# Performance work log

Measured on AMD Instinct MI355X. Metric: run time of the kernel, lower is better.

Reference implementation:

```python
import jax, jax.numpy as jnp
import numpy as np

B, N, D, Y = 4, 2048, 512, 8921


def setup_inputs() -> dict:
    key = jax.random.key(0)
    ks = jax.random.split(key, 9)
    scale = 1.0 / np.sqrt(D)
    return {
        "x": jax.random.normal(ks[0], (B, N, D), jnp.float32),
        "target": (jax.random.uniform(ks[1], (B, Y), jnp.float32) > 0.98).astype(jnp.float32),
        "y_flow": jax.random.normal(ks[2], (B, Y), jnp.float32),
        "U_w": jax.random.normal(ks[3], (Y, D), jnp.float32) * scale,
        "Ug_w": jax.random.normal(ks[4], (Y, D), jnp.float32) * scale,
        "final_w": jax.random.normal(ks[5], (Y, D), jnp.float32) * scale,
        "final_b": jax.random.normal(ks[6], (Y,), jnp.float32) * scale,
        "gate_w": jax.random.normal(ks[7], (D,), jnp.float32) * scale,
        "gate_b": jax.random.normal(ks[8], (), jnp.float32) * scale,
    }


def reference(x, target, y_flow, U_w, Ug_w, final_w, final_b, gate_w, gate_b):
    # Label attention branch: alpha = softmax(U_w @ x^T) over tokens -> [B, Y, N]
    alpha = jax.nn.softmax(jnp.einsum("yd,bnd->byn", U_w, x), axis=-1)
    m = jnp.einsum("byn,bnd->byd", alpha, x)  # [B, Y, D]

    # Gate attention branch
    alpha_g = jax.nn.softmax(jnp.einsum("yd,bnd->byn", Ug_w, x), axis=-1)
    m_g = jnp.einsum("byn,bnd->byd", alpha_g, x)  # [B, Y, D]

    # gate = tanh(Linear(D,1)(m_gate)) -> [B, Y]
    gate = jnp.tanh(jnp.einsum("byd,d->by", m_g, gate_w) + gate_b)

    # y = sum_d(final_w * m) + final_b + y_flow * gate
    y = jnp.einsum("yd,byd->by", final_w, m) + final_b + y_flow * gate

    # BCEWithLogitsLoss (mean): logaddexp(0, y) - y * target, numerically stable
    loss = jnp.mean(jnp.logaddexp(0.0, y) - y * target)
    return (y, loss)
```

## Files before the change

kernel.cpp:

```cpp
#include <hip/hip_runtime.h>
#include <stdint.h>

#define BQ 4
#define NQ 2048
#define DQ 512
#define YQ 8921
#define YGRP 140
#define NH 4
#define NCHQ 32
#define NUNITS (YGRP * BQ * NH)
#define NLP 140
#define GXOFF 65536
#define L2E 1.44269504088896340736f

typedef __attribute__((ext_vector_type(8))) short bf16x8;
typedef __attribute__((ext_vector_type(4))) float f32x4;

__device__ inline short f2bf(float f) {
  unsigned u = __float_as_uint(f);
  u += 0x7fffu + ((u >> 16) & 1u);
  return (short)(u >> 16);
}

__device__ inline bf16x8 pack8(float4 a, float4 b) {
  bf16x8 h;
  h[0] = f2bf(a.x); h[1] = f2bf(a.y); h[2] = f2bf(a.z); h[3] = f2bf(a.w);
  h[4] = f2bf(b.x); h[5] = f2bf(b.y); h[6] = f2bf(b.z); h[7] = f2bf(b.w);
  return h;
}

__device__ inline void gl_lds16(const void* g, void* l) {
  __builtin_amdgcn_global_load_lds((const __attribute__((address_space(1))) void*)g,
                                   (__attribute__((address_space(3))) void*)l, 16, 0, 0);
}

__global__ __launch_bounds__(256) void prep_gx(const float* __restrict__ x,
                                               const float* __restrict__ gate_w,
                                               float* __restrict__ gx) {
  int rid = blockIdx.x * 4 + (threadIdx.x >> 6);
  int lane = threadIdx.x & 63;
  const float* src = x + (size_t)rid * DQ + lane * 8;
  float4 v0 = *(const float4*)src;
  float4 v1 = *(const float4*)(src + 4);
  const float* gwp = gate_w + lane * 8;
  float s = v0.x * gwp[0] + v0.y * gwp[1] + v0.z * gwp[2] + v0.w * gwp[3]
          + v1.x * gwp[4] + v1.y * gwp[5] + v1.z * gwp[6] + v1.w * gwp[7];
#pragma unroll
  for (int d = 1; d < 64; d <<= 1) s += __shfl_xor(s, d);
  if (lane == 0) gx[rid] = s;
}

__global__ __launch_bounds__(256) void prep_xfrag(const float* __restrict__ x,
                                                  const float* __restrict__ gate_w,
                                                  char* __restrict__ ws_x2,
                                                  float* __restrict__ gx) {
  __shared__ float xs[16 * 512];
  int t = blockIdx.x;
  const float* src = x + ((size_t)t << 13);
  int tid = threadIdx.x;
#pragma unroll
  for (int i = 0; i < 8; ++i)
    *(float4*)(xs + i * 1024 + tid * 4) = *(const float4*)(src + i * 1024 + tid * 4);
  __syncthreads();
  char* dst = ws_x2 + ((size_t)t << 14);
#pragma unroll
  for (int i = 0; i < 4; ++i) {
    int s = i * 256 + tid;
    int l = s & 63, kk = s >> 6;
    int row = l & 15, g = l >> 4;
    const float* p = xs + row * 512 + kk * 32 + g * 8;
    *(bf16x8*)(dst + s * 16) = pack8(*(const float4*)p, *(const float4*)(p + 4));
  }
  int row = tid >> 4, sub = tid & 15;
  const float* xr = xs + row * 512 + sub * 32;
  const float* gw = gate_w + sub * 32;
  float s = 0.f;
#pragma unroll
  for (int i = 0; i < 8; ++i) {
    float4 a = *(const float4*)(xr + i * 4);
    float4 g = *(const float4*)(gw + i * 4);
    s += a.x * g.x + a.y * g.y + a.z * g.z + a.w * g.w;
  }
  s += __shfl_xor(s, 1); s += __shfl_xor(s, 2);
  s += __shfl_xor(s, 4); s += __shfl_xor(s, 8);
  if (sub == 0) gx[t * 16 + row] = s;
}

__global__ __launch_bounds__(256) void prep_w(const float* __restrict__ Uw,
                                              const float* __restrict__ Gw,
                                              const float* __restrict__ Fw,
                                              char* __restrict__ ws_w) {
  int rid = blockIdx.x * 4 + (threadIdx.x >> 6);
  if (rid >= 3 * YQ) return;
  int lane = threadIdx.x & 63;
  int mat = rid / YQ, y = rid % YQ;
  const float* src = (mat == 0 ? Uw : (mat == 1 ? Gw : Fw)) + (size_t)y * DQ + lane * 8;
  *(bf16x8*)(ws_w + (size_t)rid * 1024 + lane * 16) =
      pack8(*(const float4*)src, *(const float4*)(src + 4));
}

template<bool FULL>
__global__ __launch_bounds__(256, 2) void fused_kernel(
    const float* __restrict__ x, const char* __restrict__ ws_x2,
    const char* __restrict__ ws_w,
    const float* __restrict__ Uw, const float* __restrict__ Gw,
    const float* __restrict__ Fw, const float* __restrict__ gx,
    float4* __restrict__ ws_state) {
  extern __shared__ char smem[];
  const int tid = threadIdx.x, l = tid & 63, w = tid >> 6;
  const int lr = l & 15, lg4 = l >> 4;
  int u = (blockIdx.x & 7) * (NUNITS / 8) + (blockIdx.x >> 3);
  const int b = u / (YGRP * NH);
  const int r0 = u % (YGRP * NH);
  const int yg = r0 / NH, nh = r0 % NH;
  const int ybase = yg * 64 + w * 16;
  const int nbase = nh * (NQ / NH);

  bf16x8 wU[16], wG[16], wF[16];
  {
    int y = ybase + lr; if (y >= YQ) y = YQ - 1;
    if constexpr (FULL) {
      const char* p0 = ws_w + ((size_t)y * DQ + lg4 * 8) * 2;
#pragma unroll
      for (int kk = 0; kk < 16; ++kk) {
        wU[kk] = *(const bf16x8*)(p0 + kk * 64);
        wG[kk] = *(const bf16x8*)(p0 + (size_t)YQ * 1024 + kk * 64);
        wF[kk] = *(const bf16x8*)(p0 + (size_t)YQ * 2048 + kk * 64);
      }
    } else {
      const float* pu = Uw + (size_t)y * DQ + lg4 * 8;
      const float* pg = Gw + (size_t)y * DQ + lg4 * 8;
      const float* pf = Fw + (size_t)y * DQ + lg4 * 8;
#pragma unroll
      for (int kk = 0; kk < 16; ++kk) {
        wU[kk] = pack8(*(const float4*)(pu + kk * 32), *(const float4*)(pu + kk * 32 + 4));
        wG[kk] = pack8(*(const float4*)(pg + kk * 32), *(const float4*)(pg + kk * 32 + 4));
        wF[kk] = pack8(*(const float4*)(pf + kk * 32), *(const float4*)(pf + kk * 32 + 4));
      }
    }
  }

  float lU = 0.f, aU = 0.f, lG = 0.f, aG = 0.f;

  if constexpr (FULL) {
    *(float2*)(smem + GXOFF + tid * 8) = *(const float2*)(gx + b * NQ + nbase + tid * 2);
    const char* xb = ws_x2 + (((size_t)(b * 128 + nh * 32)) << 14);
    auto stage = [&](int c) {
      const char* src = xb + ((size_t)c << 14);
      char* lb = smem + (c & 3) * 16384;
#pragma unroll
      for (int j = 0; j < 4; ++j) {
        int s = w * 4 + j;
        gl_lds16(src + s * 1024 + l * 16, lb + s * 1024);
      }
    };
    auto mfma_only = [&](int c, f32x4& sU, f32x4& sG, f32x4& sF) {
      const char* ab = smem + (c & 3) * 16384 + l * 16;
#pragma unroll
      for (int r = 0; r < 4; ++r) { sU[r] = 0.f; sG[r] = 0.f; sF[r] = 0.f; }
      __builtin_amdgcn_s_setprio(1);
#pragma unroll
      for (int kk = 0; kk < 16; ++kk) {
        bf16x8 a = *(const bf16x8*)(ab + kk * 1024);
        sU = __builtin_amdgcn_mfma_f32_16x16x32_bf16(a, wU[kk], sU, 0, 0, 0);
        sG = __builtin_amdgcn_mfma_f32_16x16x32_bf16(a, wG[kk], sG, 0, 0, 0);
        sF = __builtin_amdgcn_mfma_f32_16x16x32_bf16(a, wF[kk], sF, 0, 0, 0);
      }
      __builtin_amdgcn_s_setprio(0);
    };
    auto tail = [&](int c, const f32x4& sU, const f32x4& sG, const f32x4& sF) {
      float4 gxv = *(const float4*)(smem + GXOFF + c * 64 + lg4 * 16);
      float gv[4] = {gxv.x, gxv.y, gxv.z, gxv.w};
#pragma unroll
      for (int r = 0; r < 4; ++r) {
        float eu = __builtin_amdgcn_exp2f(sU[r] * L2E);
        lU += eu; aU = fmaf(eu, sF[r], aU);
        float eg = __builtin_amdgcn_exp2f(sG[r] * L2E);
        lG += eg; aG = fmaf(eg, gv[r], aG);
      }
    };

    __syncthreads();
    stage(0); stage(1);
    asm volatile("s_waitcnt vmcnt(4)" ::: "memory");
    __builtin_amdgcn_s_barrier();

    f32x4 pU, pG, pF, qU, qG, qF;
    mfma_only(0, pU, pG, pF);

#pragma unroll 1
    for (int cp = 0; cp < 15; ++cp) {
      const int c0 = 2 * cp;
      stage(c0 + 2); stage(c0 + 3);
      asm volatile("s_waitcnt vmcnt(8)" ::: "memory");
      __builtin_amdgcn_sched_barrier(0);
      __builtin_amdgcn_s_barrier();
      mfma_only(c0 + 1, qU, qG, qF);
      tail(c0, pU, pG, pF);
      asm volatile("s_waitcnt vmcnt(4)" ::: "memory");
      __builtin_amdgcn_sched_barrier(0);
      __builtin_amdgcn_s_barrier();
      mfma_only(c0 + 2, pU, pG, pF);
      tail(c0 + 1, qU, qG, qF);
    }
    asm volatile("s_waitcnt vmcnt(0)" ::: "memory");
    __builtin_amdgcn_sched_barrier(0);
    __builtin_amdgcn_s_barrier();
    mfma_only(31, qU, qG, qF);
    tail(30, pU, pG, pF);
    tail(31, qU, qG, qF);
  } else {
    const float* gxb = gx + b * NQ + nbase + lg4 * 4;
    for (int c = 0; c < NCHQ; ++c) {
      __syncthreads();
#pragma unroll
      for (int j = 0; j < 4; ++j) {
        int slot = j * 256 + tid;
        int kk = slot >> 6, l2 = slot & 63;
        int row = l2 & 15, g4 = l2 >> 4;
        const float* g = x + ((size_t)(b * NQ + nbase + c * 16 + row)) * DQ
                       + kk * 32 + g4 * 8;
        *(bf16x8*)(smem + slot * 16) = pack8(*(const float4*)g, *(const float4*)(g + 4));
      }
      __syncthreads();
      const char* ab = smem + l * 16;
      f32x4 sU = {0.f, 0.f, 0.f, 0.f}, sG = sU, sF = sU;
#pragma unroll
      for (int kk = 0; kk < 16; ++kk) {
        bf16x8 a = *(const bf16x8*)(ab + kk * 1024);
        sU = __builtin_amdgcn_mfma_f32_16x16x32_bf16(a, wU[kk], sU, 0, 0, 0);
        sG = __builtin_amdgcn_mfma_f32_16x16x32_bf16(a, wG[kk], sG, 0, 0, 0);
        sF = __builtin_amdgcn_mfma_f32_16x16x32_bf16(a, wF[kk], sF, 0, 0, 0);
      }
      float4 gxv = *(const float4*)(gxb + c * 16);
      float gv[4] = {gxv.x, gxv.y, gxv.z, gxv.w};
#pragma unroll
      for (int r = 0; r < 4; ++r) {
        float eu = __builtin_amdgcn_exp2f(sU[r] * L2E);
        lU += eu; aU = fmaf(eu, sF[r], aU);
        float eg = __builtin_amdgcn_exp2f(sG[r] * L2E);
        lG += eg; aG = fmaf(eg, gv[r], aG);
      }
    }
  }

#pragma unroll
  for (int d = 16; d < 64; d <<= 1) {
    lU += __shfl_xor(lU, d); aU += __shfl_xor(aU, d);
    lG += __shfl_xor(lG, d); aG += __shfl_xor(aG, d);
  }

  int y = ybase + lr;
  if (lg4 == 0 && y < YQ) {
    float4 st; st.x = lU; st.y = aU; st.z = lG; st.w = aG;
    ws_state[(size_t)(b * NH + nh) * YQ + y] = st;
  }
}

__global__ __launch_bounds__(256) void merge_kernel(
    const float4* __restrict__ ws_state, const float* __restrict__ fb,
    const float* __restrict__ gate_b, const float* __restrict__ yflow,
    const float* __restrict__ target, float* __restrict__ out_y,
    float* __restrict__ loss_part) {
  __shared__ float sb[256];
  int t = blockIdx.x * 256 + threadIdx.x;
  float lt = 0.f;
  if (t < BQ * YQ) {
    int b = t / YQ, y = t % YQ;
    float lU = 0.f, aU = 0.f, lG = 0.f, aG = 0.f;
#pragma unroll
    for (int nh = 0; nh < NH; ++nh) {
      float4 s = ws_state[(size_t)(b * NH + nh) * YQ + y];
      lU += s.x; aU += s.y; lG += s.z; aG += s.w;
    }
    float gate = tanhf(aG / lG + gate_b[0]);
    float yv = aU / lU + fb[y] + yflow[t] * gate;
    out_y[t] = yv;
    float tg = target[t];
    lt = fmaxf(yv, 0.f) + log1pf(__expf(-fabsf(yv))) - yv * tg;
  }
  sb[threadIdx.x] = lt;
  __syncthreads();
  for (int st = 128; st > 0; st >>= 1) {
    if (threadIdx.x < st) sb[threadIdx.x] += sb[threadIdx.x + st];
    __syncthreads();
  }
  if (threadIdx.x == 0) loss_part[blockIdx.x] = sb[0];
}

__global__ __launch_bounds__(256) void loss_kernel(const float* __restrict__ lp,
                                                   float* __restrict__ out) {
  __shared__ float sb[256];
  float s = (threadIdx.x < NLP) ? lp[threadIdx.x] : 0.f;
  sb[threadIdx.x] = s;
  __syncthreads();
  for (int st = 128; st > 0; st >>= 1) {
    if (threadIdx.x < st) sb[threadIdx.x] += sb[threadIdx.x + st];
    __syncthreads();
  }
  if (threadIdx.x == 0) out[BQ * YQ] = sb[0] / (float)(BQ * YQ);
}

extern "C" void kernel_launch(void* const* d_in, const int* in_sizes, int n_in,
                              void* d_out, int out_size, void* d_ws, size_t ws_size,
                              hipStream_t stream) {
  const float* x      = (const float*)d_in[0];
  const float* target = (const float*)d_in[1];
  const float* yflow  = (const float*)d_in[2];
  const float* Uw     = (const float*)d_in[3];
  const float* Gw     = (const float*)d_in[4];
  const float* Fw     = (const float*)d_in[5];
  const float* fb     = (const float*)d_in[6];
  const float* gw     = (const float*)d_in[7];
  const float* gb     = (const float*)d_in[8];
  float* out = (float*)d_out;
  char* ws = (char*)d_ws;

  const size_t xbytes  = (size_t)BQ * NQ * DQ * 2;
  const size_t wbytes  = (size_t)3 * YQ * DQ * 2;
  const size_t gxbytes = (size_t)BQ * NQ * 4;
  const size_t stbytes = (size_t)BQ * NH * YQ * 16;
  const size_t lpbytes = (size_t)NLP * 4;
  const bool full = ws_size >= xbytes + wbytes + gxbytes + stbytes + lpbytes;

  char* ws_x2; char* ws_w; float* gxp; float4* stp; float* lp;
  if (full) {
    ws_x2 = ws; ws_w = ws + xbytes;
    gxp = (float*)(ws + xbytes + wbytes);
    stp = (float4*)(ws + xbytes + wbytes + gxbytes);
    lp  = (float*)(ws + xbytes + wbytes + gxbytes + stbytes);
  } else {
    ws_x2 = nullptr; ws_w = nullptr;
    gxp = (float*)ws;
    stp = (float4*)(ws + gxbytes);
    lp  = (float*)(ws + gxbytes + stbytes);
  }

  (void)hipFuncSetAttribute(reinterpret_cast<const void*>(&fused_kernel<true>),
                            hipFuncAttributeMaxDynamicSharedMemorySize, 67584);
  (void)hipFuncSetAttribute(reinterpret_cast<const void*>(&fused_kernel<false>),
                            hipFuncAttributeMaxDynamicSharedMemorySize, 16384);

  if (full) {
    prep_xfrag<<<dim3(BQ * 128), 256, 0, stream>>>(x, gw, ws_x2, gxp);
    prep_w<<<dim3((3 * YQ + 3) / 4), 256, 0, stream>>>(Uw, Gw, Fw, ws_w);
    fused_kernel<true ><<<dim3(NUNITS), 256, 67584, stream>>>(
        x, ws_x2, ws_w, Uw, Gw, Fw, gxp, stp);
  } else {
    prep_gx<<<dim3(2048), 256, 0, stream>>>(x, gw, gxp);
    fused_kernel<false><<<dim3(NUNITS), 256, 16384, stream>>>(
        x, ws_x2, ws_w, Uw, Gw, Fw, gxp, stp);
  }
  merge_kernel<<<dim3(NLP), 256, 0, stream>>>(stp, fb, gb, yflow, target, out, lp);
  loss_kernel<<<1, 256, 0, stream>>>(lp, out);
}
```

Baseline: 219.7 us.

## Double per-wave label tile, halve token split, and drop weight prep kernel

Each wave now holds two 16-label tiles (128 labels per block) of register-resident U/Ug/final weights and reuses each shared-memory x fragment across six MFMAs, while the token range is split eight ways instead of four. The separate bf16 weight-conversion kernel is removed and weights are converted from fp32 inline when loaded. The double-buffered MFMA/tail software pipeline is replaced by a simpler loop with prefetch two chunks ahead. The aim is to cut x traffic per label and one launch, at the cost of double the weight registers, occupancy lowered to one block per CU, and less overlap between MFMA and exp work.

Measured after the change: 810.3 us. 3.69x slower.

```diff
diff --git a/kernel.cpp b/kernel.cpp
--- a/kernel.cpp
+++ b/kernel.cpp
@@ -5,9 +5,9 @@
 #define NQ 2048
 #define DQ 512
 #define YQ 8921
-#define YGRP 140
-#define NH 4
-#define NCHQ 32
+#define YGRP 70
+#define NH 8
+#define NCHQ 16
 #define NUNITS (YGRP * BQ * NH)
 #define NLP 140
 #define GXOFF 65536
@@ -86,23 +86,9 @@
   if (sub == 0) gx[t * 16 + row] = s;
 }
 
-__global__ __launch_bounds__(256) void prep_w(const float* __restrict__ Uw,
-                                              const float* __restrict__ Gw,
-                                              const float* __restrict__ Fw,
-                                              char* __restrict__ ws_w) {
-  int rid = blockIdx.x * 4 + (threadIdx.x >> 6);
-  if (rid >= 3 * YQ) return;
-  int lane = threadIdx.x & 63;
-  int mat = rid / YQ, y = rid % YQ;
-  const float* src = (mat == 0 ? Uw : (mat == 1 ? Gw : Fw)) + (size_t)y * DQ + lane * 8;
-  *(bf16x8*)(ws_w + (size_t)rid * 1024 + lane * 16) =
-      pack8(*(const float4*)src, *(const float4*)(src + 4));
-}
-
 template<bool FULL>
-__global__ __launch_bounds__(256, 2) void fused_kernel(
+__global__ __launch_bounds__(256, 1) void fused_kernel(
     const float* __restrict__ x, const char* __restrict__ ws_x2,
-    const char* __restrict__ ws_w,
     const float* __restrict__ Uw, const float* __restrict__ Gw,
     const float* __restrict__ Fw, const float* __restrict__ gx,
     float4* __restrict__ ws_state) {
@@ -113,38 +99,32 @@
   const int b = u / (YGRP * NH);
   const int r0 = u % (YGRP * NH);
   const int yg = r0 / NH, nh = r0 % NH;
-  const int ybase = yg * 64 + w * 16;
+  const int ybase = yg * 128 + w * 32;
   const int nbase = nh * (NQ / NH);
 
-  bf16x8 wU[16], wG[16], wF[16];
-  {
-    int y = ybase + lr; if (y >= YQ) y = YQ - 1;
-    if constexpr (FULL) {
-      const char* p0 = ws_w + ((size_t)y * DQ + lg4 * 8) * 2;
-#pragma unroll
-      for (int kk = 0; kk < 16; ++kk) {
-        wU[kk] = *(const bf16x8*)(p0 + kk * 64);
-        wG[kk] = *(const bf16x8*)(p0 + (size_t)YQ * 1024 + kk * 64);
-        wF[kk] = *(const bf16x8*)(p0 + (size_t)YQ * 2048 + kk * 64);
-      }
-    } else {
-      const float* pu = Uw + (size_t)y * DQ + lg4 * 8;
-      const float* pg = Gw + (size_t)y * DQ + lg4 * 8;
-      const float* pf = Fw + (size_t)y * DQ + lg4 * 8;
-#pragma unroll
-      for (int kk = 0; kk < 16; ++kk) {
-        wU[kk] = pack8(*(const float4*)(pu + kk * 32), *(const float4*)(pu + kk * 32 + 4));
-        wG[kk] = pack8(*(const float4*)(pg + kk * 32), *(const float4*)(pg + kk * 32 + 4));
-        wF[kk] = pack8(*(const float4*)(pf + kk * 32), *(const float4*)(pf + kk * 32 + 4));
-      }
-    }
-  }
-
-  float lU = 0.f, aU = 0.f, lG = 0.f, aG = 0.f;
+  bf16x8 wU[2][16], wG[2][16], wF[2][16];
+#pragma unroll
+  for (int t = 0; t < 2; ++t) {
+    int y = ybase + t * 16 + lr; if (y >= YQ) y = YQ - 1;
+    const float* pu = Uw + (size_t)y * DQ + lg4 * 8;
+    const float* pg = Gw + (size_t)y * DQ + lg4 * 8;
+    const float* pf = Fw + (size_t)y * DQ + lg4 * 8;
+#pragma unroll
+    for (int kk = 0; kk < 16; ++kk) {
+      wU[t][kk] = pack8(*(const float4*)(pu + kk * 32), *(const float4*)(pu + kk * 32 + 4));
+      wG[t][kk] = pack8(*(const float4*)(pg + kk * 32), *(const float4*)(pg + kk * 32 + 4));
+      wF[t][kk] = pack8(*(const float4*)(pf + kk * 32), *(const float4*)(pf + kk * 32 + 4));
+    }
+  }
+
+  float lU0 = 0.f, aU0 = 0.f, lG0 = 0.f, aG0 = 0.f;
+  float lU1 = 0.f, aU1 = 0.f, lG1 = 0.f, aG1 = 0.f;
 
   if constexpr (FULL) {
-    *(float2*)(smem + GXOFF + tid * 8) = *(const float2*)(gx + b * NQ + nbase + tid * 2);
-    const char* xb = ws_x2 + (((size_t)(b * 128 + nh * 32)) << 14);
+    ((float*)(smem + GXOFF))[tid] = gx[b * NQ + nbase + tid];
+    __syncthreads();
+
+    const char* xb = ws_x2 + (((size_t)(b * 128 + nh * NCHQ)) << 14);
     auto stage = [&](int c) {
       const char* src = xb + ((size_t)c << 14);
       char* lb = smem + (c & 3) * 16384;
@@ -154,61 +134,49 @@
         gl_lds16(src + s * 1024 + l * 16, lb + s * 1024);
       }
     };
-    auto mfma_only = [&](int c, f32x4& sU, f32x4& sG, f32x4& sF) {
+    auto compute = [&](int c) {
       const char* ab = smem + (c & 3) * 16384 + l * 16;
-#pragma unroll
-      for (int r = 0; r < 4; ++r) { sU[r] = 0.f; sG[r] = 0.f; sF[r] = 0.f; }
+      f32x4 sU0 = {0.f, 0.f, 0.f, 0.f}, sG0 = sU0, sF0 = sU0;
+      f32x4 sU1 = sU0, sG1 = sU0, sF1 = sU0;
       __builtin_amdgcn_s_setprio(1);
 #pragma unroll
       for (int kk = 0; kk < 16; ++kk) {
         bf16x8 a = *(const bf16x8*)(ab + kk * 1024);
-        sU = __builtin_amdgcn_mfma_f32_16x16x32_bf16(a, wU[kk], sU, 0, 0, 0);
-        sG = __builtin_amdgcn_mfma_f32_16x16x32_bf16(a, wG[kk], sG, 0, 0, 0);
-        sF = __builtin_amdgcn_mfma_f32_16x16x32_bf16(a, wF[kk], sF, 0, 0, 0);
+        sU0 = __builtin_amdgcn_mfma_f32_16x16x32_bf16(a, wU[0][kk], sU0, 0, 0, 0);
+        sG0 = __builtin_amdgcn_mfma_f32_16x16x32_bf16(a, wG[0][kk], sG0, 0, 0, 0);
+        sF0 = __builtin_amdgcn_mfma_f32_16x16x32_bf16(a, wF[0][kk], sF0, 0, 0, 0);
+        sU1 = __builtin_amdgcn_mfma_f32_16x16x32_bf16(a, wU[1][kk], sU1, 0, 0, 0);
+        sG1 = __builtin_amdgcn_mfma_f32_16x16x32_bf16(a, wG[1][kk], sG1, 0, 0, 0);
+        sF1 = __builtin_amdgcn_mfma_f32_16x16x32_bf16(a, wF[1][kk], sF1, 0, 0, 0);
       }
       __builtin_amdgcn_s_setprio(0);
-    };
-    auto tail = [&](int c, const f32x4& sU, const f32x4& sG, const f32x4& sF) {
       float4 gxv = *(const float4*)(smem + GXOFF + c * 64 + lg4 * 16);
       float gv[4] = {gxv.x, gxv.y, gxv.z, gxv.w};
 #pragma unroll
       for (int r = 0; r < 4; ++r) {
-        float eu = __builtin_amdgcn_exp2f(sU[r] * L2E);
-        lU += eu; aU = fmaf(eu, sF[r], aU);
-        float eg = __builtin_amdgcn_exp2f(sG[r] * L2E);
-        lG += eg; aG = fmaf(eg, gv[r], aG);
+        float e;
+        e = __builtin_amdgcn_exp2f(sU0[r] * L2E); lU0 += e; aU0 = fmaf(e, sF0[r], aU0);
+        e = __builtin_amdgcn_exp2f(sG0[r] * L2E); lG0 += e; aG0 = fmaf(e, gv[r], aG0);
+        e = __builtin_amdgcn_exp2f(sU1[r] * L2E); lU1 += e; aU1 = fmaf(e, sF1[r], aU1);
+        e = __builtin_amdgcn_exp2f(sG1[r] * L2E); lG1 += e; aG1 = fmaf(e, gv[r], aG1);
       }
     };
 
-    __syncthreads();
     stage(0); stage(1);
     asm volatile("s_waitcnt vmcnt(4)" ::: "memory");
     __builtin_amdgcn_s_barrier();
 
-    f32x4 pU, pG, pF, qU, qG, qF;
-    mfma_only(0, pU, pG, pF);
-
 #pragma unroll 1
-    for (int cp = 0; cp < 15; ++cp) {
-      const int c0 = 2 * cp;
-      stage(c0 + 2); stage(c0 + 3);
-      asm volatile("s_waitcnt vmcnt(8)" ::: "memory");
-      __builtin_amdgcn_sched_barrier(0);
-      __builtin_amdgcn_s_barrier();
-      mfma_only(c0 + 1, qU, qG, qF);
-      tail(c0, pU, pG, pF);
-      asm volatile("s_waitcnt vmcnt(4)" ::: "memory");
-      __builtin_amdgcn_sched_barrier(0);
-      __builtin_amdgcn_s_barrier();
-      mfma_only(c0 + 2, pU, pG, pF);
-      tail(c0 + 1, qU, qG, qF);
-    }
-    asm volatile("s_waitcnt vmcnt(0)" ::: "memory");
-    __builtin_amdgcn_sched_barrier(0);
-    __builtin_amdgcn_s_barrier();
-    mfma_only(31, qU, qG, qF);
-    tail(30, pU, pG, pF);
-    tail(31, qU, qG, qF);
+    for (int c = 0; c < NCHQ; ++c) {
+      if (c + 2 < NCHQ) stage(c + 2);
+      compute(c);
+      if (c + 1 < NCHQ) {
+        if (c + 2 < NCHQ) asm volatile("s_waitcnt vmcnt(4)" ::: "memory");
+        else              asm volatile("s_waitcnt vmcnt(0)" ::: "memory");
+        __builtin_amdgcn_sched_barrier(0);
+        __builtin_amdgcn_s_barrier();
+      }
+    }
   } else {
     const float* gxb = gx + b * NQ + nbase + lg4 * 4;
     for (int c = 0; c < NCHQ; ++c) {
@@ -224,36 +192,50 @@
       }
       __syncthreads();
       const char* ab = smem + l * 16;
-      f32x4 sU = {0.f, 0.f, 0.f, 0.f}, sG = sU, sF = sU;
+      f32x4 sU0 = {0.f, 0.f, 0.f, 0.f}, sG0 = sU0, sF0 = sU0;
+      f32x4 sU1 = sU0, sG1 = sU0, sF1 = sU0;
 #pragma unroll
       for (int kk = 0; kk < 16; ++kk) {
         bf16x8 a = *(const bf16x8*)(ab + kk * 1024);
-        sU = __builtin_amdgcn_mfma_f32_16x16x32_bf16(a, wU[kk], sU, 0, 0, 0);
-        sG = __builtin_amdgcn_mfma_f32_16x16x32_bf16(a, wG[kk], sG, 0, 0, 0);
-        sF = __builtin_amdgcn_mfma_f32_16x16x32_bf16(a, wF[kk], sF, 0, 0, 0);
+        sU0 = __builtin_amdgcn_mfma_f32_16x16x32_bf16(a, wU[0][kk], sU0, 0, 0, 0);
+        sG0 = __builtin_amdgcn_mfma_f32_16x16x32_bf16(a, wG[0][kk], sG0, 0, 0, 0);
+        sF0 = __builtin_amdgcn_mfma_f32_16x16x32_bf16(a, wF[0][kk], sF0, 0, 0, 0);
+        sU1 = __builtin_amdgcn_mfma_f32_16x16x32_bf16(a, wU[1][kk], sU1, 0, 0, 0);
+        sG1 = __builtin_amdgcn_mfma_f32_16x16x32_bf16(a, wG[1][kk], sG1, 0, 0, 0);
+        sF1 = __builtin_amdgcn_mfma_f32_16x16x32_bf16(a, wF[1][kk], sF1, 0, 0, 0);
       }
       float4 gxv = *(const float4*)(gxb + c * 16);
       float gv[4] = {gxv.x, gxv.y, gxv.z, gxv.w};
 #pragma unroll
       for (int r = 0; r < 4; ++r) {
-        float eu = __builtin_amdgcn_exp2f(sU[r] * L2E);
-        lU += eu; aU = fmaf(eu, sF[r], aU);
-        float eg = __builtin_amdgcn_exp2f(sG[r] * L2E);
-        lG += eg; aG = fmaf(eg, gv[r], aG);
+        float e;
+        e = __builtin_amdgcn_exp2f(sU0[r] * L2E); lU0 += e; aU0 = fmaf(e, sF0[r], aU0);
+        e = __builtin_amdgcn_exp2f(sG0[r] * L2E); lG0 += e; aG0 = fmaf(e, gv[r], aG0);
+        e = __builtin_amdgcn_exp2f(sU1[r] * L2E); lU1 += e; aU1 = fmaf(e, sF1[r], aU1);
+        e = __builtin_amdgcn_exp2f(sG1[r] * L2E); lG1 += e; aG1 = fmaf(e, gv[r], aG1);
       }
     }
   }
 
 #pragma unroll
   for (int d = 16; d < 64; d <<= 1) {
-    lU += __shfl_xor(lU, d); aU += __shfl_xor(aU, d);
-    lG += __shfl_xor(lG, d); aG += __shfl_xor(aG, d);
-  }
-
-  int y = ybase + lr;
-  if (lg4 == 0 && y < YQ) {
-    float4 st; st.x = lU; st.y = aU; st.z = lG; st.w = aG;
-    ws_state[(size_t)(b * NH + nh) * YQ + y] = st;
+    lU0 += __shfl_xor(lU0, d); aU0 += __shfl_xor(aU0, d);
+    lG0 += __shfl_xor(lG0, d); aG0 += __shfl_xor(aG0, d);
+    lU1 += __shfl_xor(lU1, d); aU1 += __shfl_xor(aU1, d);
+    lG1 += __shfl_xor(lG1, d); aG1 += __shfl_xor(aG1, d);
+  }
+
+  if (lg4 == 0) {
+    int y0 = ybase + lr;
+    if (y0 < YQ) {
+      float4 st; st.x = lU0; st.y = aU0; st.z = lG0; st.w = aG0;
+      ws_state[(size_t)(b * NH + nh) * YQ + y0] = st;
+    }
+    int y1 = ybase + 16 + lr;
+    if (y1 < YQ) {
+      float4 st; st.x = lU1; st.y = aU1; st.z = lG1; st.w = aG1;
+      ws_state[(size_t)(b * NH + nh) * YQ + y1] = st;
+    }
   }
 }
 
@@ -317,39 +299,37 @@
   char* ws = (char*)d_ws;
 
   const size_t xbytes  = (size_t)BQ * NQ * DQ * 2;
-  const size_t wbytes  = (size_t)3 * YQ * DQ * 2;
   const size_t gxbytes = (size_t)BQ * NQ * 4;
   const size_t stbytes = (size_t)BQ * NH * YQ * 16;
   const size_t lpbytes = (size_t)NLP * 4;
-  const bool full = ws_size >= xbytes + wbytes + gxbytes + stbytes + lpbytes;
-
-  char* ws_x2; char* ws_w; float* gxp; float4* stp; float* lp;
+  const bool full = ws_size >= xbytes + gxbytes + stbytes + lpbytes;
+
+  char* ws_x2; float* gxp; float4* stp; float* lp;
   if (full) {
-    ws_x2 = ws; ws_w = ws + xbytes;
-    gxp = (float*)(ws + xbytes + wbytes);
-    stp = (float4*)(ws + xbytes + wbytes + gxbytes);
-    lp  = (float*)(ws + xbytes + wbytes + gxbytes + stbytes);
+    ws_x2 = ws;
+    gxp = (float*)(ws + xbytes);
+    stp = (float4*)(ws + xbytes + gxbytes);
+    lp  = (float*)(ws + xbytes + gxbytes + stbytes);
   } else {
-    ws_x2 = nullptr; ws_w = nullptr;
+    ws_x2 = nullptr;
     gxp = (float*)ws;
     stp = (float4*)(ws + gxbytes);
     lp  = (float*)(ws + gxbytes + stbytes);
   }
 
   (void)hipFuncSetAttribute(reinterpret_cast<const void*>(&fused_kernel<true>),
-                            hipFuncAttributeMaxDynamicSharedMemorySize, 67584);
+                            hipFuncAttributeMaxDynamicSharedMemorySize, 66560);
   (void)hipFuncSetAttribute(reinterpret_cast<const void*>(&fused_kernel<false>),
                             hipFuncAttributeMaxDynamicSharedMemorySize, 16384);
 
   if (full) {
     prep_xfrag<<<dim3(BQ * 128), 256, 0, stream>>>(x, gw, ws_x2, gxp);
-    prep_w<<<dim3((3 * YQ + 3) / 4), 256, 0, stream>>>(Uw, Gw, Fw, ws_w);
-    fused_kernel<true ><<<dim3(NUNITS), 256, 67584, stream>>>(
-        x, ws_x2, ws_w, Uw, Gw, Fw, gxp, stp);
+    fused_kernel<true ><<<dim3(NUNITS), 256, 66560, stream>>>(
+        x, ws_x2, Uw, Gw, Fw, gxp, stp);
   } else {
     prep_gx<<<dim3(2048), 256, 0, stream>>>(x, gw, gxp);
     fused_kernel<false><<<dim3(NUNITS), 256, 16384, stream>>>(
-        x, ws_x2, ws_w, Uw, Gw, Fw, gxp, stp);
+        x, ws_x2, Uw, Gw, Fw, gxp, stp);
   }
   merge_kernel<<<dim3(NLP), 256, 0, stream>>>(stp, fb, gb, yflow, target, out, lp);
   loss_kernel<<<1, 256, 0, stream>>>(lp, out);
```

## Drop weight prep kernel, double chunk size, register-prefetch A fragments

Applied to the files above, without the earlier changes.

Removes the prep_w kernel, so the fused kernel converts the fp32 U/Ug/final weights to bf16 in its prologue. Chunks grow from 16 to 32 tokens with 32KB LDS stages (128KB ring), and each half-chunk's A fragments are read from LDS into registers ahead of its MFMAs so reads overlap compute. The goal is to cut an extra launch plus the weight write/read traffic and halve the barrier count. The cost is one block per CU instead of two and much higher register pressure from two 16-entry A arrays, which risks spilling.

Result: slower. 393.6 us (+79.1%).

```diff
diff --git a/kernel.cpp b/kernel.cpp
--- a/kernel.cpp
+++ b/kernel.cpp
@@ -7,10 +7,10 @@
 #define YQ 8921
 #define YGRP 140
 #define NH 4
-#define NCHQ 32
+#define NCHQ 16
 #define NUNITS (YGRP * BQ * NH)
 #define NLP 140
-#define GXOFF 65536
+#define GXOFF 131072
 #define L2E 1.44269504088896340736f
 
 typedef __attribute__((ext_vector_type(8))) short bf16x8;
@@ -86,23 +86,9 @@
   if (sub == 0) gx[t * 16 + row] = s;
 }
 
-__global__ __launch_bounds__(256) void prep_w(const float* __restrict__ Uw,
-                                              const float* __restrict__ Gw,
-                                              const float* __restrict__ Fw,
-                                              char* __restrict__ ws_w) {
-  int rid = blockIdx.x * 4 + (threadIdx.x >> 6);
-  if (rid >= 3 * YQ) return;
-  int lane = threadIdx.x & 63;
-  int mat = rid / YQ, y = rid % YQ;
-  const float* src = (mat == 0 ? Uw : (mat == 1 ? Gw : Fw)) + (size_t)y * DQ + lane * 8;
-  *(bf16x8*)(ws_w + (size_t)rid * 1024 + lane * 16) =
-      pack8(*(const float4*)src, *(const float4*)(src + 4));
-}
-
 template<bool FULL>
-__global__ __launch_bounds__(256, 2) void fused_kernel(
+__global__ __launch_bounds__(256, 1) void fused_kernel(
     const float* __restrict__ x, const char* __restrict__ ws_x2,
-    const char* __restrict__ ws_w,
     const float* __restrict__ Uw, const float* __restrict__ Gw,
     const float* __restrict__ Fw, const float* __restrict__ gx,
     float4* __restrict__ ws_state) {
@@ -119,24 +105,14 @@
   bf16x8 wU[16], wG[16], wF[16];
   {
     int y = ybase + lr; if (y >= YQ) y = YQ - 1;
-    if constexpr (FULL) {
-      const char* p0 = ws_w + ((size_t)y * DQ + lg4 * 8) * 2;
-#pragma unroll
-      for (int kk = 0; kk < 16; ++kk) {
-        wU[kk] = *(const bf16x8*)(p0 + kk * 64);
-        wG[kk] = *(const bf16x8*)(p0 + (size_t)YQ * 1024 + kk * 64);
-        wF[kk] = *(const bf16x8*)(p0 + (size_t)YQ * 2048 + kk * 64);
-      }
-    } else {
-      const float* pu = Uw + (size_t)y * DQ + lg4 * 8;
-      const float* pg = Gw + (size_t)y * DQ + lg4 * 8;
-      const float* pf = Fw + (size_t)y * DQ + lg4 * 8;
-#pragma unroll
-      for (int kk = 0; kk < 16; ++kk) {
-        wU[kk] = pack8(*(const float4*)(pu + kk * 32), *(const float4*)(pu + kk * 32 + 4));
-        wG[kk] = pack8(*(const float4*)(pg + kk * 32), *(const float4*)(pg + kk * 32 + 4));
-        wF[kk] = pack8(*(const float4*)(pf + kk * 32), *(const float4*)(pf + kk * 32 + 4));
-      }
+    const float* pu = Uw + (size_t)y * DQ + lg4 * 8;
+    const float* pg = Gw + (size_t)y * DQ + lg4 * 8;
+    const float* pf = Fw + (size_t)y * DQ + lg4 * 8;
+#pragma unroll
+    for (int kk = 0; kk < 16; ++kk) {
+      wU[kk] = pack8(*(const float4*)(pu + kk * 32), *(const float4*)(pu + kk * 32 + 4));
+      wG[kk] = pack8(*(const float4*)(pg + kk * 32), *(const float4*)(pg + kk * 32 + 4));
+      wF[kk] = pack8(*(const float4*)(pf + kk * 32), *(const float4*)(pf + kk * 32 + 4));
     }
   }
 
@@ -144,32 +120,34 @@
 
   if constexpr (FULL) {
     *(float2*)(smem + GXOFF + tid * 8) = *(const float2*)(gx + b * NQ + nbase + tid * 2);
+    __syncthreads();
+
     const char* xb = ws_x2 + (((size_t)(b * 128 + nh * 32)) << 14);
     auto stage = [&](int c) {
-      const char* src = xb + ((size_t)c << 14);
-      char* lb = smem + (c & 3) * 16384;
-#pragma unroll
-      for (int j = 0; j < 4; ++j) {
-        int s = w * 4 + j;
-        gl_lds16(src + s * 1024 + l * 16, lb + s * 1024);
+      char* lb = smem + (c & 3) * 32768;
+#pragma unroll
+      for (int j = 0; j < 8; ++j) {
+        int s = w * 8 + j;
+        gl_lds16(xb + (((size_t)(2 * c + (s >> 4))) << 14) + (s & 15) * 1024 + l * 16,
+                 lb + s * 1024);
       }
     };
-    auto mfma_only = [&](int c, f32x4& sU, f32x4& sG, f32x4& sF) {
-      const char* ab = smem + (c & 3) * 16384 + l * 16;
-#pragma unroll
-      for (int r = 0; r < 4; ++r) { sU[r] = 0.f; sG[r] = 0.f; sF[r] = 0.f; }
+    auto read16 = [&](int c, int t2, bf16x8* A) {
+      const char* ab = smem + (c & 3) * 32768 + t2 * 16384 + l * 16;
+#pragma unroll
+      for (int kk = 0; kk < 16; ++kk) A[kk] = *(const bf16x8*)(ab + kk * 1024);
+    };
+    auto mfma48 = [&](const bf16x8* A, int c, int t2) {
+      f32x4 sU = {0.f, 0.f, 0.f, 0.f}, sG = sU, sF = sU;
       __builtin_amdgcn_s_setprio(1);
 #pragma unroll
       for (int kk = 0; kk < 16; ++kk) {
-        bf16x8 a = *(const bf16x8*)(ab + kk * 1024);
-        sU = __builtin_amdgcn_mfma_f32_16x16x32_bf16(a, wU[kk], sU, 0, 0, 0);
-        sG = __builtin_amdgcn_mfma_f32_16x16x32_bf16(a, wG[kk], sG, 0, 0, 0);
-        sF = __builtin_amdgcn_mfma_f32_16x16x32_bf16(a, wF[kk], sF, 0, 0, 0);
+        sU = __builtin_amdgcn_mfma_f32_16x16x32_bf16(A[kk], wU[kk], sU, 0, 0, 0);
+        sG = __builtin_amdgcn_mfma_f32_16x16x32_bf16(A[kk], wG[kk], sG, 0, 0, 0);
+        sF = __builtin_amdgcn_mfma_f32_16x16x32_bf16(A[kk], wF[kk], sF, 0, 0, 0);
       }
       __builtin_amdgcn_s_setprio(0);
-    };
-    auto tail = [&](int c, const f32x4& sU, const f32x4& sG, const f32x4& sF) {
-      float4 gxv = *(const float4*)(smem + GXOFF + c * 64 + lg4 * 16);
+      float4 gxv = *(const float4*)(smem + GXOFF + c * 128 + t2 * 64 + lg4 * 16);
       float gv[4] = {gxv.x, gxv.y, gxv.z, gxv.w};
 #pragma unroll
       for (int r = 0; r < 4; ++r) {
@@ -180,66 +158,61 @@
       }
     };
 
-    __syncthreads();
+    bf16x8 Aa[16], Ab[16];
     stage(0); stage(1);
-    asm volatile("s_waitcnt vmcnt(4)" ::: "memory");
+    asm volatile("s_waitcnt vmcnt(8)" ::: "memory");
     __builtin_amdgcn_s_barrier();
-
-    f32x4 pU, pG, pF, qU, qG, qF;
-    mfma_only(0, pU, pG, pF);
+    read16(0, 0, Aa);
 
 #pragma unroll 1
-    for (int cp = 0; cp < 15; ++cp) {
-      const int c0 = 2 * cp;
-      stage(c0 + 2); stage(c0 + 3);
-      asm volatile("s_waitcnt vmcnt(8)" ::: "memory");
+    for (int c = 0; c < NCHQ - 1; ++c) {
+      if (c + 2 < NCHQ) stage(c + 2);
+      read16(c, 1, Ab);
+      mfma48(Aa, c, 0);
+      if (c + 2 < NCHQ) asm volatile("s_waitcnt vmcnt(8)" ::: "memory");
+      else              asm volatile("s_waitcnt vmcnt(0)" ::: "memory");
       __builtin_amdgcn_sched_barrier(0);
       __builtin_amdgcn_s_barrier();
-      mfma_only(c0 + 1, qU, qG, qF);
-      tail(c0, pU, pG, pF);
-      asm volatile("s_waitcnt vmcnt(4)" ::: "memory");
-      __builtin_amdgcn_sched_barrier(0);
-      __builtin_amdgcn_s_barrier();
-      mfma_only(c0 + 2, pU, pG, pF);
-      tail(c0 + 1, qU, qG, qF);
+      read16(c + 1, 0, Aa);
+      mfma48(Ab, c, 1);
     }
-    asm volatile("s_waitcnt vmcnt(0)" ::: "memory");
-    __builtin_amdgcn_sched_barrier(0);
-    __builtin_amdgcn_s_barrier();
-    mfma_only(31, qU, qG, qF);
-    tail(30, pU, pG, pF);
-    tail(31, qU, qG, qF);
+    read16(NCHQ - 1, 1, Ab);
+    mfma48(Aa, NCHQ - 1, 0);
+    mfma48(Ab, NCHQ - 1, 1);
   } else {
     const float* gxb = gx + b * NQ + nbase + lg4 * 4;
     for (int c = 0; c < NCHQ; ++c) {
       __syncthreads();
 #pragma unroll
-      for (int j = 0; j < 4; ++j) {
+      for (int j = 0; j < 8; ++j) {
         int slot = j * 256 + tid;
-        int kk = slot >> 6, l2 = slot & 63;
-        int row = l2 & 15, g4 = l2 >> 4;
-        const float* g = x + ((size_t)(b * NQ + nbase + c * 16 + row)) * DQ
+        int t2 = slot >> 10, kk = (slot >> 6) & 15, l2 = slot & 63;
+        int row = t2 * 16 + (l2 & 15), g4 = l2 >> 4;
+        const float* g = x + ((size_t)(b * NQ + nbase + c * 32 + row)) * DQ
                        + kk * 32 + g4 * 8;
         *(bf16x8*)(smem + slot * 16) = pack8(*(const float4*)g, *(const float4*)(g + 4));
       }
       __syncthreads();
-      const char* ab = smem + l * 16;
-      f32x4 sU = {0.f, 0.f, 0.f, 0.f}, sG = sU, sF = sU;
-#pragma unroll
-      for (int kk = 0; kk < 16; ++kk) {
-        bf16x8 a = *(const bf16x8*)(ab + kk * 1024);
-        sU = __builtin_amdgcn_mfma_f32_16x16x32_bf16(a, wU[kk], sU, 0, 0, 0);
-        sG = __builtin_amdgcn_mfma_f32_16x16x32_bf16(a, wG[kk], sG, 0, 0, 0);
-        sF = __builtin_amdgcn_mfma_f32_16x16x32_bf16(a, wF[kk], sF, 0, 0, 0);
-      }
-      float4 gxv = *(const float4*)(gxb + c * 16);
-      float gv[4] = {gxv.x, gxv.y, gxv.z, gxv.w};
-#pragma unroll
-      for (int r = 0; r < 4; ++r) {
-        float eu = __builtin_amdgcn_exp2f(sU[r] * L2E);
-        lU += eu; aU = fmaf(eu, sF[r], aU);
-        float eg = __builtin_amdgcn_exp2f(sG[r] * L2E);
-        lG += eg; aG = fmaf(eg, gv[r], aG);
+#pragma unroll
+      for (int t2 = 0; t2 < 2; ++t2) {
+        const char* ab = smem + t2 * 16384 + l * 16;
+        f32x4 sU = {0.f, 0.f, 0.f, 0.f}, sG = sU, sF = sU;
+#pragma unroll
+        for (int kk = 0; kk < 16; ++kk) {
+          bf16x8 a = *(const bf16x8*)(ab + kk * 1024);
+          sU = __builtin_amdgcn_mfma_f32_16x16x32_bf16(a, wU[kk], sU, 0, 0, 0);
+          sG = __builtin_amdgcn_mfma_f32_16x16x32_bf16(a, wG[kk], sG, 0, 0, 0);
+          sF = __builtin_amdgcn_mfma_f32_16x16x32_bf16(a, wF[kk], sF, 0, 0, 0);
+        }
+        float4 gxv = *(const float4*)(gxb + c * 32 + t2 * 16);
+        float gv[4] = {gxv.x, gxv.y, gxv.z, gxv.w};
+#pragma unroll
+        for (int r = 0; r < 4; ++r) {
+          float eu = __builtin_amdgcn_exp2f(sU[r] * L2E);
+          lU += eu; aU = fmaf(eu, sF[r], aU);
+          float eg = __builtin_amdgcn_exp2f(sG[r] * L2E);
+          lG += eg; aG = fmaf(eg, gv[r], aG);
+        }
       }
     }
   }
@@ -317,39 +290,37 @@
   char* ws = (char*)d_ws;
 
   const size_t xbytes  = (size_t)BQ * NQ * DQ * 2;
-  const size_t wbytes  = (size_t)3 * YQ * DQ * 2;
   const size_t gxbytes = (size_t)BQ * NQ * 4;
   const size_t stbytes = (size_t)BQ * NH * YQ * 16;
   const size_t lpbytes = (size_t)NLP * 4;
-  const bool full = ws_size >= xbytes + wbytes + gxbytes + stbytes + lpbytes;
-
-  char* ws_x2; char* ws_w; float* gxp; float4* stp; float* lp;
+  const bool full = ws_size >= xbytes + gxbytes + stbytes + lpbytes;
+
+  char* ws_x2; float* gxp; float4* stp; float* lp;
   if (full) {
-    ws_x2 = ws; ws_w = ws + xbytes;
-    gxp = (float*)(ws + xbytes + wbytes);
-    stp = (float4*)(ws + xbytes + wbytes + gxbytes);
-    lp  = (float*)(ws + xbytes + wbytes + gxbytes + stbytes);
+    ws_x2 = ws;
+    gxp = (float*)(ws + xbytes);
+    stp = (float4*)(ws + xbytes + gxbytes);
+    lp  = (float*)(ws + xbytes + gxbytes + stbytes);
   } else {
-    ws_x2 = nullptr; ws_w = nullptr;
+    ws_x2 = nullptr;
     gxp = (float*)ws;
     stp = (float4*)(ws + gxbytes);
     lp  = (float*)(ws + gxbytes + stbytes);
   }
 
   (void)hipFuncSetAttribute(reinterpret_cast<const void*>(&fused_kernel<true>),
-                            hipFuncAttributeMaxDynamicSharedMemorySize, 67584);
+                            hipFuncAttributeMaxDynamicSharedMemorySize, 133120);
   (void)hipFuncSetAttribute(reinterpret_cast<const void*>(&fused_kernel<false>),
-                            hipFuncAttributeMaxDynamicSharedMemorySize, 16384);
+                            hipFuncAttributeMaxDynamicSharedMemorySize, 32768);
 
   if (full) {
     prep_xfrag<<<dim3(BQ * 128), 256, 0, stream>>>(x, gw, ws_x2, gxp);
-    prep_w<<<dim3((3 * YQ + 3) / 4), 256, 0, stream>>>(Uw, Gw, Fw, ws_w);
-    fused_kernel<true ><<<dim3(NUNITS), 256, 67584, stream>>>(
-        x, ws_x2, ws_w, Uw, Gw, Fw, gxp, stp);
+    fused_kernel<true ><<<dim3(NUNITS), 256, 133120, stream>>>(
+        x, ws_x2, Uw, Gw, Fw, gxp, stp);
   } else {
     prep_gx<<<dim3(2048), 256, 0, stream>>>(x, gw, gxp);
-    fused_kernel<false><<<dim3(NUNITS), 256, 16384, stream>>>(
-        x, ws_x2, ws_w, Uw, Gw, Fw, gxp, stp);
+    fused_kernel<false><<<dim3(NUNITS), 256, 32768, stream>>>(
+        x, ws_x2, Uw, Gw, Fw, gxp, stp);
   }
   merge_kernel<<<dim3(NLP), 256, 0, stream>>>(stp, fb, gb, yflow, target, out, lp);
   loss_kernel<<<1, 256, 0, stream>>>(lp, out);
```

## Give each wave a private LDS double buffer and drop block barriers

Applied to the files above, without the earlier changes.

Previously the four waves shared a four-slot LDS ring filled cooperatively, so every chunk needed a block-wide s_barrier. Now each wave stages only the x fragments it consumes into its own 16KB region, split into two half-chunks, and synchronises with waitcnt alone. The gate-x values also get a per-wave copy. This removes inter-wave barriers, but each wave now loads the same shared x tile redundantly, which multiplies global/L2 traffic and LDS footprint, and the prefetch depth drops to one half-chunk with no pipelining of the exp tail.

Result: slower. 272.4 us (+24.0%).

```diff
diff --git a/kernel.cpp b/kernel.cpp
--- a/kernel.cpp
+++ b/kernel.cpp
@@ -140,107 +140,91 @@
     }
   }
 
+  char* mybuf = smem + w * 16384;
+  char* gxa   = smem + GXOFF + w * 2048;
+
   float lU = 0.f, aU = 0.f, lG = 0.f, aG = 0.f;
+  f32x4 sU, sG, sF;
+
+  {
+    const float4* gsrc = (const float4*)(gx + b * NQ + nbase);
+    *(float4*)(gxa + l * 32)      = gsrc[l * 2];
+    *(float4*)(gxa + l * 32 + 16) = gsrc[l * 2 + 1];
+  }
+
+  auto computeHalf = [&](int s) {
+    const char* ab = mybuf + (s & 1) * 8192 + l * 16;
+    const int kb = (s & 1) * 8;
+    __builtin_amdgcn_s_setprio(1);
+#pragma unroll
+    for (int kk = 0; kk < 8; ++kk) {
+      bf16x8 a = *(const bf16x8*)(ab + kk * 1024);
+      sU = __builtin_amdgcn_mfma_f32_16x16x32_bf16(a, wU[kb + kk], sU, 0, 0, 0);
+      sG = __builtin_amdgcn_mfma_f32_16x16x32_bf16(a, wG[kb + kk], sG, 0, 0, 0);
+      sF = __builtin_amdgcn_mfma_f32_16x16x32_bf16(a, wF[kb + kk], sF, 0, 0, 0);
+    }
+    __builtin_amdgcn_s_setprio(0);
+  };
+  auto tail = [&](int c) {
+    float4 gxv = *(const float4*)(gxa + c * 64 + lg4 * 16);
+    float gv[4] = {gxv.x, gxv.y, gxv.z, gxv.w};
+#pragma unroll
+    for (int r = 0; r < 4; ++r) {
+      float eu = __builtin_amdgcn_exp2f(sU[r] * L2E);
+      lU += eu; aU = fmaf(eu, sF[r], aU);
+      float eg = __builtin_amdgcn_exp2f(sG[r] * L2E);
+      lG += eg; aG = fmaf(eg, gv[r], aG);
+    }
+  };
 
   if constexpr (FULL) {
-    *(float2*)(smem + GXOFF + tid * 8) = *(const float2*)(gx + b * NQ + nbase + tid * 2);
     const char* xb = ws_x2 + (((size_t)(b * 128 + nh * 32)) << 14);
-    auto stage = [&](int c) {
-      const char* src = xb + ((size_t)c << 14);
-      char* lb = smem + (c & 3) * 16384;
-#pragma unroll
-      for (int j = 0; j < 4; ++j) {
-        int s = w * 4 + j;
-        gl_lds16(src + s * 1024 + l * 16, lb + s * 1024);
+    auto stage = [&](int s) {
+      const char* src = xb + (((size_t)(s >> 1)) << 14) + (s & 1) * 8192;
+      char* lb = mybuf + (s & 1) * 8192;
+#pragma unroll
+      for (int j = 0; j < 8; ++j)
+        gl_lds16(src + j * 1024 + l * 16, lb + j * 1024);
+    };
+
+    stage(0); stage(1);
+#pragma unroll 1
+    for (int c = 0; c < NCHQ; ++c) {
+      const int s0 = 2 * c, s1 = 2 * c + 1;
+      asm volatile("s_waitcnt vmcnt(8)" ::: "memory");
+#pragma unroll
+      for (int r = 0; r < 4; ++r) { sU[r] = 0.f; sG[r] = 0.f; sF[r] = 0.f; }
+      computeHalf(s0);
+      asm volatile("s_waitcnt lgkmcnt(0)" ::: "memory");
+      if (s0 + 2 < 2 * NCHQ) stage(s0 + 2);
+      if (s1 < 2 * NCHQ - 1) asm volatile("s_waitcnt vmcnt(8)" ::: "memory");
+      else                   asm volatile("s_waitcnt vmcnt(0)" ::: "memory");
+      computeHalf(s1);
+      asm volatile("s_waitcnt lgkmcnt(0)" ::: "memory");
+      if (s1 + 2 < 2 * NCHQ) stage(s1 + 2);
+      tail(c);
+    }
+  } else {
+#pragma unroll 1
+    for (int c = 0; c < NCHQ; ++c) {
+#pragma unroll
+      for (int h = 0; h < 2; ++h) {
+        char* lb = mybuf + h * 8192;
+#pragma unroll
+        for (int kk = 0; kk < 8; ++kk) {
+          int row = l & 15, g4 = l >> 4;
+          const float* g = x + ((size_t)(b * NQ + nbase + c * 16 + row)) * DQ
+                         + (h * 8 + kk) * 32 + g4 * 8;
+          *(bf16x8*)(lb + kk * 1024 + l * 16) =
+              pack8(*(const float4*)g, *(const float4*)(g + 4));
+        }
+        if (h == 0) {
+#pragma unroll
+          for (int r = 0; r < 4; ++r) { sU[r] = 0.f; sG[r] = 0.f; sF[r] = 0.f; }
+        }
+        computeHalf(h);
       }
-    };
-    auto mfma_only = [&](int c, f32x4& sU, f32x4& sG, f32x4& sF) {
-      const char* ab = smem + (c & 3) * 16384 + l * 16;
-#pragma unroll
-      for (int r = 0; r < 4; ++r) { sU[r] = 0.f; sG[r] = 0.f; sF[r] = 0.f; }
-      __builtin_amdgcn_s_setprio(1);
-#pragma unroll
-      for (int kk = 0; kk < 16; ++kk) {
-        bf16x8 a = *(const bf16x8*)(ab + kk * 1024);
-        sU = __builtin_amdgcn_mfma_f32_16x16x32_bf16(a, wU[kk], sU, 0, 0, 0);
-        sG = __builtin_amdgcn_mfma_f32_16x16x32_bf16(a, wG[kk], sG, 0, 0, 0);
-        sF = __builtin_amdgcn_mfma_f32_16x16x32_bf16(a, wF[kk], sF, 0, 0, 0);
-      }
-      __builtin_amdgcn_s_setprio(0);
-    };
-    auto tail = [&](int c, const f32x4& sU, const f32x4& sG, const f32x4& sF) {
-      float4 gxv = *(const float4*)(smem + GXOFF + c * 64 + lg4 * 16);
-      float gv[4] = {gxv.x, gxv.y, gxv.z, gxv.w};
-#pragma unroll
-      for (int r = 0; r < 4; ++r) {
-        float eu = __builtin_amdgcn_exp2f(sU[r] * L2E);
-        lU += eu; aU = fmaf(eu, sF[r], aU);
-        float eg = __builtin_amdgcn_exp2f(sG[r] * L2E);
-        lG += eg; aG = fmaf(eg, gv[r], aG);
-      }
-    };
-
-    __syncthreads();
-    stage(0); stage(1);
-    asm volatile("s_waitcnt vmcnt(4)" ::: "memory");
-    __builtin_amdgcn_s_barrier();
-
-    f32x4 pU, pG, pF, qU, qG, qF;
-    mfma_only(0, pU, pG, pF);
-
-#pragma unroll 1
-    for (int cp = 0; cp < 15; ++cp) {
-      const int c0 = 2 * cp;
-      stage(c0 + 2); stage(c0 + 3);
-      asm volatile("s_waitcnt vmcnt(8)" ::: "memory");
-      __builtin_amdgcn_sched_barrier(0);
-      __builtin_amdgcn_s_barrier();
-      mfma_only(c0 + 1, qU, qG, qF);
-      tail(c0, pU, pG, pF);
-      asm volatile("s_waitcnt vmcnt(4)" ::: "memory");
-      __builtin_amdgcn_sched_barrier(0);
-      __builtin_amdgcn_s_barrier();
-      mfma_only(c0 + 2, pU, pG, pF);
-      tail(c0 + 1, qU, qG, qF);
-    }
-    asm volatile("s_waitcnt vmcnt(0)" ::: "memory");
-    __builtin_amdgcn_sched_barrier(0);
-    __builtin_amdgcn_s_barrier();
-    mfma_only(31, qU, qG, qF);
-    tail(30, pU, pG, pF);
-    tail(31, qU, qG, qF);
-  } else {
-    const float* gxb = gx + b * NQ + nbase + lg4 * 4;
-    for (int c = 0; c < NCHQ; ++c) {
-      __syncthreads();
-#pragma unroll
-      for (int j = 0; j < 4; ++j) {
-        int slot = j * 256 + tid;
-        int kk = slot >> 6, l2 = slot & 63;
-        int row = l2 & 15, g4 = l2 >> 4;
-        const float* g = x + ((size_t)(b * NQ + nbase + c * 16 + row)) * DQ
-                       + kk * 32 + g4 * 8;
-        *(bf16x8*)(smem + slot * 16) = pack8(*(const float4*)g, *(const float4*)(g + 4));
-      }
-      __syncthreads();
-      const char* ab = smem + l * 16;
-      f32x4 sU = {0.f, 0.f, 0.f, 0.f}, sG = sU, sF = sU;
-#pragma unroll
-      for (int kk = 0; kk < 16; ++kk) {
-        bf16x8 a = *(const bf16x8*)(ab + kk * 1024);
-        sU = __builtin_amdgcn_mfma_f32_16x16x32_bf16(a, wU[kk], sU, 0, 0, 0);
-        sG = __builtin_amdgcn_mfma_f32_16x16x32_bf16(a, wG[kk], sG, 0, 0, 0);
-        sF = __builtin_amdgcn_mfma_f32_16x16x32_bf16(a, wF[kk], sF, 0, 0, 0);
-      }
-      float4 gxv = *(const float4*)(gxb + c * 16);
-      float gv[4] = {gxv.x, gxv.y, gxv.z, gxv.w};
-#pragma unroll
-      for (int r = 0; r < 4; ++r) {
-        float eu = __builtin_amdgcn_exp2f(sU[r] * L2E);
-        lU += eu; aU = fmaf(eu, sF[r], aU);
-        float eg = __builtin_amdgcn_exp2f(sG[r] * L2E);
-        lG += eg; aG = fmaf(eg, gv[r], aG);
-      }
+      tail(c);
     }
   }
 
@@ -337,18 +321,18 @@
   }
 
   (void)hipFuncSetAttribute(reinterpret_cast<const void*>(&fused_kernel<true>),
-                            hipFuncAttributeMaxDynamicSharedMemorySize, 67584);
+                            hipFuncAttributeMaxDynamicSharedMemorySize, 73728);
   (void)hipFuncSetAttribute(reinterpret_cast<const void*>(&fused_kernel<false>),
-                            hipFuncAttributeMaxDynamicSharedMemorySize, 16384);
+                            hipFuncAttributeMaxDynamicSharedMemorySize, 73728);
 
   if (full) {
     prep_xfrag<<<dim3(BQ * 128), 256, 0, stream>>>(x, gw, ws_x2, gxp);
     prep_w<<<dim3((3 * YQ + 3) / 4), 256, 0, stream>>>(Uw, Gw, Fw, ws_w);
-    fused_kernel<true ><<<dim3(NUNITS), 256, 67584, stream>>>(
+    fused_kernel<true ><<<dim3(NUNITS), 256, 73728, stream>>>(
         x, ws_x2, ws_w, Uw, Gw, Fw, gxp, stp);
   } else {
     prep_gx<<<dim3(2048), 256, 0, stream>>>(x, gw, gxp);
-    fused_kernel<false><<<dim3(NUNITS), 256, 16384, stream>>>(
+    fused_kernel<false><<<dim3(NUNITS), 256, 73728, stream>>>(
         x, ws_x2, ws_w, Uw, Gw, Fw, gxp, stp);
   }
   merge_kernel<<<dim3(NLP), 256, 0, stream>>>(stp, fb, gb, yflow, target, out, lp);
```
